# Performance work log

Hardware: AMD Instinct MI355X
Metric: run time of the kernel (lower is better)

The kernel has to match this reference:

```python
import jax, jax.numpy as jnp
import numpy as np

B, S, L, D = 4, 8, 350, 768  # paragraphs, sentences/paragraph, padded pair length, hidden
P = B * S * (S - 1)          # number of ordered sentence pairs = 224

# pair p -> (z, j, k): same enumeration order as the torch nested loops
_IDX = np.array([(z, j, k) for z in range(B) for j in range(S) for k in range(S) if j != k])
# each pair contributes its first-sentence embedding to segment (z,j) and second to (z,k)
_SEG = np.stack([_IDX[:, 0] * S + _IDX[:, 1], _IDX[:, 0] * S + _IDX[:, 2]], axis=1).reshape(-1)  # [2P]


def setup_inputs() -> dict:
    key = jax.random.key(0)
    ks = jax.random.split(key, 8)
    sc = 0.02
    all_output = jax.random.normal(ks[0], (P, L, D), dtype=jnp.float32)
    first_sep = jax.random.randint(ks[1], (P,), 5, 150).astype(jnp.int32)           # > 1
    second_sep = (first_sep + jax.random.randint(ks[2], (P,), 5, 150)).astype(jnp.int32)  # > first_sep+1, < L
    W1 = jax.random.normal(ks[3], (D, D), dtype=jnp.float32) * sc
    b1 = jnp.zeros((D,), jnp.float32)
    v1 = jax.random.normal(ks[4], (D,), dtype=jnp.float32) * sc
    vb1 = jnp.zeros((), jnp.float32)
    W2 = jax.random.normal(ks[5], (D, D), dtype=jnp.float32) * sc
    b2 = jnp.zeros((D,), jnp.float32)
    v2 = jax.random.normal(ks[6], (D,), dtype=jnp.float32) * sc
    vb2 = jnp.zeros((), jnp.float32)
    return {"all_output": all_output, "first_sep": first_sep, "second_sep": second_sep,
            "W1": W1, "b1": b1, "v1": v1, "vb1": vb1,
            "W2": W2, "b2": b2, "v2": v2, "vb2": vb2}


def reference(all_output, first_sep, second_sep, W1, b1, v1, vb1, W2, b2, v2, vb2):
    # pair_embeddings = [CLS] token of every pair
    pair_embeddings = all_output[:, 0, :]  # [P, D]

    # ---- level one: masked attention pooling over word positions ----
    u = jnp.tanh(all_output @ W1 + b1)          # [P, L, D]
    scores = u @ v1 + vb1                       # [P, L]
    pos = jnp.arange(L)[None, :]                # [1, L]
    mask1 = (pos >= 1) & (pos < first_sep[:, None])                 # tokens 1..first_sep-1
    mask2 = (pos > first_sep[:, None]) & (pos < second_sep[:, None])  # first_sep+1..second_sep-1

    def pool(mask):
        s = jnp.where(mask, scores, -jnp.inf)
        w = jax.nn.softmax(s, axis=1)           # [P, L]
        return jnp.einsum('pl,pld->pd', w, all_output)

    e1 = pool(mask1)                            # [P, D] first-sentence embeddings
    e2 = pool(mask2)                            # [P, D] second-sentence embeddings
    emb = jnp.stack([e1, e2], axis=1).reshape(2 * P, D)  # [2P, D]

    # ---- level two: segment attention pooling per (paragraph, sentence) group ----
    seg = jnp.asarray(_SEG)                     # [2P] segment ids, num_segments = B*S
    u2 = jnp.tanh(emb @ W2 + b2)                # [2P, D]
    sc = u2 @ v2 + vb2                          # [2P]
    num_seg = B * S
    smax = jax.ops.segment_max(sc, seg, num_segments=num_seg)
    ex = jnp.exp(sc - smax[seg])
    denom = jax.ops.segment_sum(ex, seg, num_segments=num_seg)
    w = ex / denom[seg]                         # segment softmax weights
    out2 = jax.ops.segment_sum(w[:, None] * emb, seg, num_segments=num_seg).reshape(B, S, D)
    return (pair_embeddings, out2)
```

## Files before the change

kernel.cpp:

```cpp
#include <hip/hip_runtime.h>
#include <math.h>

#define LSEQ   350
#define DDIM   768
#define NPAIR  224
#define MROWS1 78400
#define NSLAB1 613
#define MAXSLAB 520

typedef short bf16x8 __attribute__((ext_vector_type(8)));
typedef float f32x4  __attribute__((ext_vector_type(4)));

typedef const unsigned int __attribute__((address_space(1)))* gas_ptr;
typedef unsigned int __attribute__((address_space(3)))* las_ptr;

__device__ __forceinline__ void gload_lds16(const void* g, void* l) {
  __builtin_amdgcn_global_load_lds((gas_ptr)g, (las_ptr)l, 16, 0, 0);
}

__device__ __forceinline__ unsigned short f2bf(float x) {
  unsigned int u = __float_as_uint(x);
  unsigned int r = (u + 0x7FFFu + ((u >> 16) & 1u)) >> 16;
  return (unsigned short)r;
}

__device__ __forceinline__ float tanh_fast(float x) {
  float e = __expf(2.f * x);
  return 1.f - 2.f / (e + 1.f);
}

__global__ __launch_bounds__(256) void k_scan(const int* __restrict__ ssep,
                                              int* __restrict__ off) {
  __shared__ int buf[256];
  const int t = threadIdx.x;
  int v = (t < NPAIR) ? (ssep[t] - 1) : 0;
  buf[t] = v;
  __syncthreads();
#pragma unroll
  for (int d = 1; d < 256; d <<= 1) {
    int add = (t >= d) ? buf[t - d] : 0;
    __syncthreads();
    buf[t] += add;
    __syncthreads();
  }
  if (t < NPAIR) off[t] = buf[t] - v;
  if (t == NPAIR - 1) off[NPAIR] = buf[t];
}

__global__ __launch_bounds__(256) void k_wt2(const float* __restrict__ W1,
                                             const float* __restrict__ W2,
                                             unsigned short* __restrict__ Wt1,
                                             unsigned short* __restrict__ Wt2) {
  const float* W = blockIdx.z ? W2 : W1;
  unsigned short* Wt = blockIdx.z ? Wt2 : Wt1;
  __shared__ float tile[32][33];
  int bk = blockIdx.x * 32, bn = blockIdx.y * 32;
  int tx = threadIdx.x & 31, ty = threadIdx.x >> 5;
#pragma unroll
  for (int i = 0; i < 32; i += 8)
    tile[ty + i][tx] = W[(size_t)(bk + ty + i) * DDIM + bn + tx];
  __syncthreads();
#pragma unroll
  for (int i = 0; i < 32; i += 8)
    Wt[(size_t)(bn + ty + i) * DDIM + bk + tx] = f2bf(tile[tx][ty + i]);
}

__global__ __launch_bounds__(256) void k_w1t(const float* __restrict__ W,
                                             unsigned short* __restrict__ Wt) {
  __shared__ float tile[32][33];
  int bk = blockIdx.x * 32, bn = blockIdx.y * 32;
  int tx = threadIdx.x & 31, ty = threadIdx.x >> 5;
#pragma unroll
  for (int i = 0; i < 32; i += 8)
    tile[ty + i][tx] = W[(size_t)(bk + ty + i) * DDIM + bn + tx];
  __syncthreads();
#pragma unroll
  for (int i = 0; i < 32; i += 8)
    Wt[(size_t)(bn + ty + i) * DDIM + bk + tx] = f2bf(tile[tx][ty + i]);
}

__global__ __launch_bounds__(256) void k_conv(const float* __restrict__ X,
                                              const int* __restrict__ ssep,
                                              const int* __restrict__ off,
                                              unsigned short* __restrict__ Xbf,
                                              int* __restrict__ rowmap) {
  const int p = blockIdx.x, tile = blockIdx.y, z = blockIdx.z;
  const int nrow = ssep[p] - 1;
  const int r0 = tile * 128 + z * 32;
  if (r0 >= nrow) return;
  const int t = threadIdx.x;
  const int o = off[p];
  if (t < 192) {
    for (int i = 0; i < 32; ++i) {
      int r = r0 + i;
      if (r >= nrow) break;
      float4 x = *(const float4*)(X + ((size_t)p * LSEQ + 1 + r) * DDIM + t * 4);
      unsigned int ux = __float_as_uint(x.x) + 0x8000u;
      unsigned int uy = __float_as_uint(x.y) + 0x8000u;
      unsigned int uz = __float_as_uint(x.z) + 0x8000u;
      unsigned int uw = __float_as_uint(x.w) + 0x8000u;
      *(uint2*)(Xbf + (size_t)(o + r) * DDIM + t * 4) =
          make_uint2(__builtin_amdgcn_perm(uy, ux, 0x07060302u),
                     __builtin_amdgcn_perm(uw, uz, 0x07060302u));
    }
  } else if (t < 224) {
    int r = r0 + (t - 192);
    if (r < nrow) rowmap[o + r] = p * LSEQ + 1 + r;
  }
}

__global__ __launch_bounds__(256, 4) void k_gemm_c(
    const unsigned short* __restrict__ Xbf, const unsigned short* __restrict__ Wt,
    const float* __restrict__ bias, const float* __restrict__ vv,
    const int* __restrict__ off, const int* __restrict__ rowmap,
    float* __restrict__ scores) {
  const int Mtotal = off[NPAIR];
  const int b = blockIdx.x;
  const int g = b / 48, r = b - g * 48;
  const int slab = g * 8 + (r & 7);
  const int nchunk = r >> 3;
  if (slab * 128 >= Mtotal) return;

  const size_t arow0 = (size_t)slab * 128;
  const int n0 = nchunk * 128;

  __shared__ unsigned short As[128 * 32];
  __shared__ unsigned short Bs[128 * 32];

  const int t = threadIdx.x;
  const int lane = t & 63, w = t >> 6;
  const int l15 = t & 15;
  const int quad = (t >> 4) & 3;
  const int wm = w >> 1, wn = w & 1;
  const int lrow = lane >> 2;
  const int lcol = (lane & 3) * 8;

  f32x4 acc[4][4];
#pragma unroll
  for (int mi = 0; mi < 4; ++mi)
#pragma unroll
    for (int ni = 0; ni < 4; ++ni)
#pragma unroll
      for (int q = 0; q < 4; ++q) acc[mi][ni][q] = 0.f;

  for (int k0 = 0; k0 < DDIM; k0 += 32) {
#pragma unroll
    for (int j = 0; j < 2; ++j) {
      int seg = w * 2 + j;
      gload_lds16(Xbf + (arow0 + seg * 16 + lrow) * DDIM + k0 + lcol, As + seg * 512);
      gload_lds16(Wt + (size_t)(n0 + seg * 16 + lrow) * DDIM + k0 + lcol, Bs + seg * 512);
    }
    __syncthreads();

    bf16x8 a[4], bfr[4];
#pragma unroll
    for (int mi = 0; mi < 4; ++mi)
      a[mi] = *(const bf16x8*)&As[(wm * 64 + mi * 16 + l15) * 32 + quad * 8];
#pragma unroll
    for (int ni = 0; ni < 4; ++ni)
      bfr[ni] = *(const bf16x8*)&Bs[(wn * 64 + ni * 16 + l15) * 32 + quad * 8];
#pragma unroll
    for (int mi = 0; mi < 4; ++mi)
#pragma unroll
      for (int ni = 0; ni < 4; ++ni)
        acc[mi][ni] = __builtin_amdgcn_mfma_f32_16x16x32_bf16(a[mi], bfr[ni], acc[mi][ni], 0, 0, 0);
    __syncthreads();
  }

  float vvv[4], bbv[4];
#pragma unroll
  for (int ni = 0; ni < 4; ++ni) {
    int n = n0 + wn * 64 + ni * 16 + l15;
    vvv[ni] = vv[n];
    bbv[ni] = bias[n];
  }
#pragma unroll
  for (int mi = 0; mi < 4; ++mi) {
#pragma unroll
    for (int reg = 0; reg < 4; ++reg) {
      float s = 0.f;
#pragma unroll
      for (int ni = 0; ni < 4; ++ni)
        s += tanh_fast(acc[mi][ni][reg] + bbv[ni]) * vvv[ni];
      s += __shfl_xor(s, 1);
      s += __shfl_xor(s, 2);
      s += __shfl_xor(s, 4);
      s += __shfl_xor(s, 8);
      if (l15 == mi * 4 + reg) {
        int row = (int)arow0 + wm * 64 + mi * 16 + quad * 4 + reg;
        if (row < Mtotal) atomicAdd(&scores[rowmap[row]], s);
      }
    }
  }
}

__global__ __launch_bounds__(256, 2) void k_gemm_score(
    const float* __restrict__ X, const unsigned short* __restrict__ Wt,
    const float* __restrict__ bias, const float* __restrict__ vv,
    float* __restrict__ outs, int Mrows, int swz) {
  int slab, nchunk;
  if (swz) {
    int b = blockIdx.x;
    int g = b / 48, r = b - g * 48;
    slab = g * 8 + (r & 7);
    nchunk = r >> 3;
    if (slab >= NSLAB1) return;
  } else {
    slab = blockIdx.y;
    nchunk = blockIdx.x;
  }
  const int row0 = slab * 128;
  const int n0 = nchunk * 128;

  __shared__ unsigned short As[128][40];
  __shared__ unsigned short Bs[128][40];

  const int t = threadIdx.x;
  const int l15 = t & 15;
  const int quad = (t >> 4) & 3;
  const int w = t >> 6;
  const int wm = w >> 1, wn = w & 1;
  const int ar = t >> 3;
  const int ac = (t & 7) * 4;
  const int br = t >> 2;
  const int bc = (t & 3) * 8;

  f32x4 acc[4][4];
#pragma unroll
  for (int mi = 0; mi < 4; ++mi)
#pragma unroll
    for (int ni = 0; ni < 4; ++ni)
#pragma unroll
      for (int q = 0; q < 4; ++q) acc[mi][ni][q] = 0.f;

  for (int k0 = 0; k0 < DDIM; k0 += 32) {
#pragma unroll
    for (int pass = 0; pass < 4; ++pass) {
      int rr = ar + pass * 32;
      int row = row0 + rr;
      float4 x = make_float4(0.f, 0.f, 0.f, 0.f);
      if (row < Mrows) x = *(const float4*)(X + (size_t)row * DDIM + k0 + ac);
      unsigned int ux = __float_as_uint(x.x) + 0x8000u;
      unsigned int uy = __float_as_uint(x.y) + 0x8000u;
      unsigned int uz = __float_as_uint(x.z) + 0x8000u;
      unsigned int uw = __float_as_uint(x.w) + 0x8000u;
      *(uint2*)&As[rr][ac] = make_uint2(__builtin_amdgcn_perm(uy, ux, 0x07060302u),
                                        __builtin_amdgcn_perm(uw, uz, 0x07060302u));
    }
#pragma unroll
    for (int pp = 0; pp < 2; ++pp) {
      int rr = br + pp * 64;
      *(uint4*)&Bs[rr][bc] = *(const uint4*)(Wt + (size_t)(n0 + rr) * DDIM + k0 + bc);
    }
    __syncthreads();

    bf16x8 a[4], bfr[4];
#pragma unroll
    for (int mi = 0; mi < 4; ++mi)
      a[mi] = *(const bf16x8*)&As[wm * 64 + mi * 16 + l15][quad * 8];
#pragma unroll
    for (int ni = 0; ni < 4; ++ni)
      bfr[ni] = *(const bf16x8*)&Bs[wn * 64 + ni * 16 + l15][quad * 8];
#pragma unroll
    for (int mi = 0; mi < 4; ++mi)
#pragma unroll
      for (int ni = 0; ni < 4; ++ni)
        acc[mi][ni] = __builtin_amdgcn_mfma_f32_16x16x32_bf16(a[mi], bfr[ni], acc[mi][ni], 0, 0, 0);
    __syncthreads();
  }

  float vvv[4], bbv[4];
#pragma unroll
  for (int ni = 0; ni < 4; ++ni) {
    int n = n0 + wn * 64 + ni * 16 + l15;
    vvv[ni] = vv[n];
    bbv[ni] = bias[n];
  }
#pragma unroll
  for (int mi = 0; mi < 4; ++mi) {
#pragma unroll
    for (int reg = 0; reg < 4; ++reg) {
      float s = 0.f;
#pragma unroll
      for (int ni = 0; ni < 4; ++ni)
        s += tanh_fast(acc[mi][ni][reg] + bbv[ni]) * vvv[ni];
      s += __shfl_xor(s, 1);
      s += __shfl_xor(s, 2);
      s += __shfl_xor(s, 4);
      s += __shfl_xor(s, 8);
      if (l15 == mi * 4 + reg) {
        int row = row0 + wm * 64 + mi * 16 + quad * 4 + reg;
        if (row < Mrows) atomicAdd(&outs[row], s);
      }
    }
  }
}

__device__ __forceinline__ float block_reduce(float v, bool is_max, float* redbuf) {
#pragma unroll
  for (int off = 1; off < 64; off <<= 1) {
    float o = __shfl_xor(v, off);
    v = is_max ? fmaxf(v, o) : (v + o);
  }
  int wv = threadIdx.x >> 6;
  if ((threadIdx.x & 63) == 0) redbuf[wv] = v;
  __syncthreads();
  float r = is_max ? fmaxf(fmaxf(redbuf[0], redbuf[1]), fmaxf(redbuf[2], redbuf[3]))
                   : (redbuf[0] + redbuf[1] + redbuf[2] + redbuf[3]);
  __syncthreads();
  return r;
}

__global__ __launch_bounds__(256) void k_pool2(
    const unsigned short* __restrict__ Xbf, const float* __restrict__ X,
    const float* __restrict__ scores, const int* __restrict__ fsep,
    const int* __restrict__ ssep, const int* __restrict__ off,
    float* __restrict__ emb, float* __restrict__ out) {
  const int p = blockIdx.x, c = blockIdx.y, t = threadIdx.x;
  const int fs = fsep[p], ss = ssep[p];
  __shared__ float sw1[LSEQ], sw2[LSEQ];
  __shared__ float redbuf[4];

  float m1p = -INFINITY, m2p = -INFINITY;
  for (int l = t; l < LSEQ; l += 256) {
    float s = scores[p * LSEQ + l];
    float s1 = (l >= 1 && l < fs) ? s : -INFINITY;
    float s2 = (l > fs && l < ss) ? s : -INFINITY;
    sw1[l] = s1; sw2[l] = s2;
    m1p = fmaxf(m1p, s1); m2p = fmaxf(m2p, s2);
  }
  __syncthreads();
  float m1 = block_reduce(m1p, true, redbuf);
  float m2 = block_reduce(m2p, true, redbuf);
  float d1p = 0.f, d2p = 0.f;
  for (int l = t; l < LSEQ; l += 256) {
    float e1v = __expf(sw1[l] - m1);
    float e2v = __expf(sw2[l] - m2);
    sw1[l] = e1v; sw2[l] = e2v;
    d1p += e1v; d2p += e2v;
  }
  __syncthreads();
  float inv1 = 1.f / block_reduce(d1p, false, redbuf);
  float inv2 = 1.f / block_reduce(d2p, false, redbuf);

  if (c == 0 && t < 192) {
    *(float4*)(out + (size_t)p * DDIM + t * 4) =
        *(const float4*)(X + (size_t)p * LSEQ * DDIM + t * 4);
  }

  if (t < 192) {
    const int o = off[p];
    float A1[4] = {0.f, 0.f, 0.f, 0.f}, A2[4] = {0.f, 0.f, 0.f, 0.f};
    for (int l = 1 + c; l < ss; l += 8) {
      float wa = sw1[l] * inv1, wb = sw2[l] * inv2;
      uint2 xv = *(const uint2*)(Xbf + (size_t)(o + l - 1) * DDIM + t * 4);
      float x0 = __uint_as_float((xv.x & 0xFFFFu) << 16);
      float x1 = __uint_as_float(xv.x & 0xFFFF0000u);
      float x2 = __uint_as_float((xv.y & 0xFFFFu) << 16);
      float x3 = __uint_as_float(xv.y & 0xFFFF0000u);
      A1[0] += wa * x0; A1[1] += wa * x1; A1[2] += wa * x2; A1[3] += wa * x3;
      A2[0] += wb * x0; A2[1] += wb * x1; A2[2] += wb * x2; A2[3] += wb * x3;
    }
    float* e1 = emb + (size_t)(2 * p) * DDIM + t * 4;
    float* e2 = emb + (size_t)(2 * p + 1) * DDIM + t * 4;
#pragma unroll
    for (int i = 0; i < 4; ++i) atomicAdd(&e1[i], A1[i]);
#pragma unroll
    for (int i = 0; i < 4; ++i) atomicAdd(&e2[i], A2[i]);
  }
}

__global__ __launch_bounds__(256) void k_pool(
    const float* __restrict__ X, const float* __restrict__ scores,
    const int* __restrict__ fsep, const int* __restrict__ ssep,
    float* __restrict__ emb, float* __restrict__ out) {
  const int p = blockIdx.x;
  const int c = blockIdx.y;
  const int t = threadIdx.x;
  const int fs = fsep[p], ss = ssep[p];
  __shared__ float sw1[LSEQ], sw2[LSEQ];
  __shared__ float redbuf[4];

  float m1p = -INFINITY, m2p = -INFINITY;
  for (int l = t; l < LSEQ; l += 256) {
    float s = scores[p * LSEQ + l];
    float s1 = (l >= 1 && l < fs) ? s : -INFINITY;
    float s2 = (l > fs && l < ss) ? s : -INFINITY;
    sw1[l] = s1; sw2[l] = s2;
    m1p = fmaxf(m1p, s1); m2p = fmaxf(m2p, s2);
  }
  __syncthreads();
  float m1 = block_reduce(m1p, true, redbuf);
  float m2 = block_reduce(m2p, true, redbuf);
  float d1p = 0.f, d2p = 0.f;
  for (int l = t; l < LSEQ; l += 256) {
    float e1v = __expf(sw1[l] - m1);
    float e2v = __expf(sw2[l] - m2);
    sw1[l] = e1v; sw2[l] = e2v;
    d1p += e1v; d2p += e2v;
  }
  __syncthreads();
  float inv1 = 1.f / block_reduce(d1p, false, redbuf);
  float inv2 = 1.f / block_reduce(d2p, false, redbuf);
  const float* base = X + (size_t)p * LSEQ * DDIM;
  if (c == 0) {
    float* po = out + (size_t)p * DDIM;
    po[t] = base[t]; po[t + 256] = base[t + 256]; po[t + 512] = base[t + 512];
  }
  if (t < 192) {
    float4 A1 = make_float4(0.f, 0.f, 0.f, 0.f);
    float4 A2 = make_float4(0.f, 0.f, 0.f, 0.f);
    for (int l = 1 + c; l < ss; l += 8) {
      float wa = sw1[l] * inv1, wb = sw2[l] * inv2;
      float4 x = *(const float4*)(base + (size_t)l * DDIM + 4 * t);
      A1.x += wa * x.x; A1.y += wa * x.y; A1.z += wa * x.z; A1.w += wa * x.w;
      A2.x += wb * x.x; A2.y += wb * x.y; A2.z += wb * x.z; A2.w += wb * x.w;
    }
    float* e1 = emb + (size_t)(2 * p) * DDIM + 4 * t;
    float* e2 = emb + (size_t)(2 * p + 1) * DDIM + 4 * t;
    atomicAdd(&e1[0], A1.x); atomicAdd(&e1[1], A1.y);
    atomicAdd(&e1[2], A1.z); atomicAdd(&e1[3], A1.w);
    atomicAdd(&e2[0], A2.x); atomicAdd(&e2[1], A2.y);
    atomicAdd(&e2[2], A2.z); atomicAdd(&e2[3], A2.w);
  }
}

__global__ __launch_bounds__(256) void k_segout(
    const float* __restrict__ emb, const float* __restrict__ sc,
    float* __restrict__ out2) {
  const int g = blockIdx.x;
  const int z = g >> 3, j = g & 7;
  const int t = threadIdx.x;
  int ee[14];
#pragma unroll
  for (int i = 0; i < 7; ++i) ee[i] = 2 * (z * 56 + j * 7 + i);
#pragma unroll
  for (int i = 0; i < 7; ++i) {
    int j2 = i + (i >= j ? 1 : 0);
    int kk = j - (j > j2 ? 1 : 0);
    ee[7 + i] = 2 * (z * 56 + j2 * 7 + kk) + 1;
  }
  float sv[14];
  float m = -INFINITY;
#pragma unroll
  for (int i = 0; i < 14; ++i) { sv[i] = sc[ee[i]]; m = fmaxf(m, sv[i]); }
  float den = 0.f;
#pragma unroll
  for (int i = 0; i < 14; ++i) { sv[i] = __expf(sv[i] - m); den += sv[i]; }
  float inv = 1.f / den;
  float a0 = 0.f, a1 = 0.f, a2 = 0.f;
#pragma unroll
  for (int i = 0; i < 14; ++i) {
    float wgt = sv[i] * inv;
    const float* er = emb + (size_t)ee[i] * DDIM;
    a0 += wgt * er[t]; a1 += wgt * er[t + 256]; a2 += wgt * er[t + 512];
  }
  out2[(size_t)g * DDIM + t] = a0;
  out2[(size_t)g * DDIM + t + 256] = a1;
  out2[(size_t)g * DDIM + t + 512] = a2;
}

extern "C" void kernel_launch(void* const* d_in, const int* in_sizes, int n_in,
                              void* d_out, int out_size, void* d_ws, size_t ws_size,
                              hipStream_t stream) {
  const float* X  = (const float*)d_in[0];
  const int* fs   = (const int*)d_in[1];
  const int* ss   = (const int*)d_in[2];
  const float* W1 = (const float*)d_in[3];
  const float* b1 = (const float*)d_in[4];
  const float* v1 = (const float*)d_in[5];
  const float* W2 = (const float*)d_in[7];
  const float* b2 = (const float*)d_in[8];
  const float* v2 = (const float*)d_in[9];
  float* out = (float*)d_out;

  char* ws = (char*)d_ws;
  const size_t XBF_ROWS = (size_t)MAXSLAB * 128 + 64;
  const size_t OFF_MAP  = XBF_ROWS * DDIM * 2;
  const size_t OFF_OFF  = OFF_MAP + XBF_ROWS * 4;
  const size_t OFF_WT1  = OFF_OFF + 1024;
  const size_t OFF_WT2  = OFF_WT1 + 1179648;
  const size_t OFF_SCORES = OFF_WT2 + 1179648;
  const size_t OFF_EMB  = OFF_SCORES + 313600;
  const size_t OFF_SC   = OFF_EMB + 1376256;
  const size_t NEED     = OFF_SC + 2048;

  if (ws_size >= NEED) {
    unsigned short* Xbf = (unsigned short*)ws;
    int*   rowmap = (int*)(ws + OFF_MAP);
    int*   off    = (int*)(ws + OFF_OFF);
    unsigned short* Wt1 = (unsigned short*)(ws + OFF_WT1);
    unsigned short* Wt2 = (unsigned short*)(ws + OFF_WT2);
    float* scores = (float*)(ws + OFF_SCORES);
    float* emb    = (float*)(ws + OFF_EMB);
    float* sc     = (float*)(ws + OFF_SC);

    k_scan<<<1, 256, 0, stream>>>(ss, off);
    k_wt2<<<dim3(24, 24, 2), 256, 0, stream>>>(W1, W2, Wt1, Wt2);
    hipMemsetAsync(scores, 0, 313600 + 1376256 + 2048, stream);
    k_conv<<<dim3(NPAIR, 3, 4), 256, 0, stream>>>(X, ss, off, Xbf, rowmap);
    k_gemm_c<<<65 * 48, 256, 0, stream>>>(Xbf, Wt1, b1, v1, off, rowmap, scores);
    k_pool2<<<dim3(NPAIR, 8), 256, 0, stream>>>(Xbf, X, scores, fs, ss, off, emb, out);
    k_gemm_score<<<dim3(6, 4), 256, 0, stream>>>(emb, Wt2, b2, v2, sc, 448, 0);
    k_segout<<<32, 256, 0, stream>>>(emb, sc, out + (size_t)NPAIR * DDIM);
  } else {
    unsigned short* Wt = (unsigned short*)ws;
    float* scores = (float*)(ws + 1179648);
    float* emb    = (float*)(ws + 1493248);
    float* sc     = scores;

    k_w1t<<<dim3(24, 24), 256, 0, stream>>>(W1, Wt);
    hipMemsetAsync(scores, 0, MROWS1 * sizeof(float), stream);
    hipMemsetAsync(emb, 0, 448 * DDIM * sizeof(float), stream);
    k_gemm_score<<<77 * 48, 256, 0, stream>>>(X, Wt, b1, v1, scores, MROWS1, 1);
    k_pool<<<dim3(NPAIR, 8), 256, 0, stream>>>(X, scores, fs, ss, emb, out);
    k_w1t<<<dim3(24, 24), 256, 0, stream>>>(W2, Wt);
    hipMemsetAsync(sc, 0, 448 * sizeof(float), stream);
    k_gemm_score<<<dim3(6, 4), 256, 0, stream>>>(emb, Wt, b2, v2, sc, 448, 0);
    k_segout<<<32, 256, 0, stream>>>(emb, sc, out + (size_t)NPAIR * DDIM);
  }
}
```

Baseline: 500.0 us.

## Merge prep kernels, store compact scores, drop rowmap, and pool without atomics

Merges the scan, the weight transposes and the zeroing of the score buffer into one prep kernel, which removes separate launches and a memset. Scores are now stored compactly by row index, so the rowmap indirection goes away. The pooling kernel uses one block per pair over all positions and writes emb directly instead of using atomics, so emb no longer needs zeroing. This gives fewer launches and less atomic traffic, but pooling now has only 224 blocks, which lowers parallelism.

```diff
diff --git a/kernel.cpp b/kernel.cpp
--- a/kernel.cpp
+++ b/kernel.cpp
@@ -29,91 +29,79 @@
   return 1.f - 2.f / (e + 1.f);
 }
 
-__global__ __launch_bounds__(256) void k_scan(const int* __restrict__ ssep,
-                                              int* __restrict__ off) {
-  __shared__ int buf[256];
+#define PREP_WT 1152
+#define PREP_ZB 263
+__global__ __launch_bounds__(256) void k_prep(
+    const float* __restrict__ W1, const float* __restrict__ W2,
+    unsigned short* __restrict__ Wt1, unsigned short* __restrict__ Wt2,
+    const int* __restrict__ ssep, int* __restrict__ off,
+    unsigned int* __restrict__ zreg) {
+  const int b = blockIdx.x;
   const int t = threadIdx.x;
-  int v = (t < NPAIR) ? (ssep[t] - 1) : 0;
-  buf[t] = v;
-  __syncthreads();
-#pragma unroll
-  for (int d = 1; d < 256; d <<= 1) {
-    int add = (t >= d) ? buf[t - d] : 0;
+  if (b < PREP_WT) {
+    const float* W = (b >= 576) ? W2 : W1;
+    unsigned short* Wt = (b >= 576) ? Wt2 : Wt1;
+    const int r = (b >= 576) ? b - 576 : b;
+    const int bk = (r % 24) * 32, bn = (r / 24) * 32;
+    __shared__ float tile[32][33];
+    const int tx = t & 31, ty = t >> 5;
+#pragma unroll
+    for (int i = 0; i < 32; i += 8)
+      tile[ty + i][tx] = W[(size_t)(bk + ty + i) * DDIM + bn + tx];
     __syncthreads();
-    buf[t] += add;
+#pragma unroll
+    for (int i = 0; i < 32; i += 8)
+      Wt[(size_t)(bn + ty + i) * DDIM + bk + tx] = f2bf(tile[tx][ty + i]);
+  } else if (b == PREP_WT) {
+    __shared__ int buf[256];
+    int v = (t < NPAIR) ? (ssep[t] - 1) : 0;
+    buf[t] = v;
     __syncthreads();
-  }
-  if (t < NPAIR) off[t] = buf[t] - v;
-  if (t == NPAIR - 1) off[NPAIR] = buf[t];
-}
-
-__global__ __launch_bounds__(256) void k_wt2(const float* __restrict__ W1,
-                                             const float* __restrict__ W2,
-                                             unsigned short* __restrict__ Wt1,
-                                             unsigned short* __restrict__ Wt2) {
-  const float* W = blockIdx.z ? W2 : W1;
-  unsigned short* Wt = blockIdx.z ? Wt2 : Wt1;
-  __shared__ float tile[32][33];
-  int bk = blockIdx.x * 32, bn = blockIdx.y * 32;
-  int tx = threadIdx.x & 31, ty = threadIdx.x >> 5;
-#pragma unroll
-  for (int i = 0; i < 32; i += 8)
-    tile[ty + i][tx] = W[(size_t)(bk + ty + i) * DDIM + bn + tx];
-  __syncthreads();
-#pragma unroll
-  for (int i = 0; i < 32; i += 8)
-    Wt[(size_t)(bn + ty + i) * DDIM + bk + tx] = f2bf(tile[tx][ty + i]);
-}
-
-__global__ __launch_bounds__(256) void k_w1t(const float* __restrict__ W,
-                                             unsigned short* __restrict__ Wt) {
-  __shared__ float tile[32][33];
-  int bk = blockIdx.x * 32, bn = blockIdx.y * 32;
-  int tx = threadIdx.x & 31, ty = threadIdx.x >> 5;
-#pragma unroll
-  for (int i = 0; i < 32; i += 8)
-    tile[ty + i][tx] = W[(size_t)(bk + ty + i) * DDIM + bn + tx];
-  __syncthreads();
-#pragma unroll
-  for (int i = 0; i < 32; i += 8)
-    Wt[(size_t)(bn + ty + i) * DDIM + bk + tx] = f2bf(tile[tx][ty + i]);
-}
-
-__global__ __launch_bounds__(256) void k_conv(const float* __restrict__ X,
+#pragma unroll
+    for (int d = 1; d < 256; d <<= 1) {
+      int add = (t >= d) ? buf[t - d] : 0;
+      __syncthreads();
+      buf[t] += add;
+      __syncthreads();
+    }
+    if (t < NPAIR) off[t] = buf[t] - v;
+    if (t == NPAIR - 1) off[NPAIR] = buf[t];
+  } else {
+    const int i = b - PREP_WT - 1;
+    zreg[(size_t)i * 256 + t] = 0u;
+  }
+}
+
+__global__ __launch_bounds__(192) void k_conv(const float* __restrict__ X,
                                               const int* __restrict__ ssep,
                                               const int* __restrict__ off,
-                                              unsigned short* __restrict__ Xbf,
-                                              int* __restrict__ rowmap) {
+                                              unsigned short* __restrict__ Xbf) {
   const int p = blockIdx.x, tile = blockIdx.y, z = blockIdx.z;
   const int nrow = ssep[p] - 1;
   const int r0 = tile * 128 + z * 32;
   if (r0 >= nrow) return;
   const int t = threadIdx.x;
   const int o = off[p];
-  if (t < 192) {
-    for (int i = 0; i < 32; ++i) {
-      int r = r0 + i;
-      if (r >= nrow) break;
-      float4 x = *(const float4*)(X + ((size_t)p * LSEQ + 1 + r) * DDIM + t * 4);
-      unsigned int ux = __float_as_uint(x.x) + 0x8000u;
-      unsigned int uy = __float_as_uint(x.y) + 0x8000u;
-      unsigned int uz = __float_as_uint(x.z) + 0x8000u;
-      unsigned int uw = __float_as_uint(x.w) + 0x8000u;
-      *(uint2*)(Xbf + (size_t)(o + r) * DDIM + t * 4) =
-          make_uint2(__builtin_amdgcn_perm(uy, ux, 0x07060302u),
-                     __builtin_amdgcn_perm(uw, uz, 0x07060302u));
-    }
-  } else if (t < 224) {
-    int r = r0 + (t - 192);
-    if (r < nrow) rowmap[o + r] = p * LSEQ + 1 + r;
+  const int rmax = min(32, nrow - r0);
+  const float* src = X + ((size_t)p * LSEQ + 1 + r0) * DDIM + t * 4;
+  unsigned short* dst = Xbf + (size_t)(o + r0) * DDIM + t * 4;
+#pragma unroll 4
+  for (int i = 0; i < rmax; ++i) {
+    float4 x = *(const float4*)(src + (size_t)i * DDIM);
+    unsigned int ux = __float_as_uint(x.x) + 0x8000u;
+    unsigned int uy = __float_as_uint(x.y) + 0x8000u;
+    unsigned int uz = __float_as_uint(x.z) + 0x8000u;
+    unsigned int uw = __float_as_uint(x.w) + 0x8000u;
+    *(uint2*)(dst + (size_t)i * DDIM) =
+        make_uint2(__builtin_amdgcn_perm(uy, ux, 0x07060302u),
+                   __builtin_amdgcn_perm(uw, uz, 0x07060302u));
   }
 }
 
 __global__ __launch_bounds__(256, 4) void k_gemm_c(
     const unsigned short* __restrict__ Xbf, const unsigned short* __restrict__ Wt,
     const float* __restrict__ bias, const float* __restrict__ vv,
-    const int* __restrict__ off, const int* __restrict__ rowmap,
-    float* __restrict__ scores) {
+    const int* __restrict__ off, float* __restrict__ scores_c) {
   const int Mtotal = off[NPAIR];
   const int b = blockIdx.x;
   const int g = b / 48, r = b - g * 48;
@@ -188,7 +176,7 @@
       s += __shfl_xor(s, 8);
       if (l15 == mi * 4 + reg) {
         int row = (int)arow0 + wm * 64 + mi * 16 + quad * 4 + reg;
-        if (row < Mtotal) atomicAdd(&scores[rowmap[row]], s);
+        if (row < Mtotal) atomicAdd(&scores_c[row], s);
       }
     }
   }
@@ -311,19 +299,20 @@
   return r;
 }
 
-__global__ __launch_bounds__(256) void k_pool2(
+__global__ __launch_bounds__(256) void k_pool3(
     const unsigned short* __restrict__ Xbf, const float* __restrict__ X,
-    const float* __restrict__ scores, const int* __restrict__ fsep,
+    const float* __restrict__ scores_c, const int* __restrict__ fsep,
     const int* __restrict__ ssep, const int* __restrict__ off,
     float* __restrict__ emb, float* __restrict__ out) {
-  const int p = blockIdx.x, c = blockIdx.y, t = threadIdx.x;
+  const int p = blockIdx.x, t = threadIdx.x;
   const int fs = fsep[p], ss = ssep[p];
+  const int o = off[p];
   __shared__ float sw1[LSEQ], sw2[LSEQ];
   __shared__ float redbuf[4];
 
   float m1p = -INFINITY, m2p = -INFINITY;
   for (int l = t; l < LSEQ; l += 256) {
-    float s = scores[p * LSEQ + l];
+    float s = (l >= 1 && l < ss) ? scores_c[o + l - 1] : 0.f;
     float s1 = (l >= 1 && l < fs) ? s : -INFINITY;
     float s2 = (l > fs && l < ss) ? s : -INFINITY;
     sw1[l] = s1; sw2[l] = s2;
@@ -343,17 +332,16 @@
   float inv1 = 1.f / block_reduce(d1p, false, redbuf);
   float inv2 = 1.f / block_reduce(d2p, false, redbuf);
 
-  if (c == 0 && t < 192) {
+  if (t < 192) {
     *(float4*)(out + (size_t)p * DDIM + t * 4) =
         *(const float4*)(X + (size_t)p * LSEQ * DDIM + t * 4);
-  }
-
-  if (t < 192) {
-    const int o = off[p];
+
     float A1[4] = {0.f, 0.f, 0.f, 0.f}, A2[4] = {0.f, 0.f, 0.f, 0.f};
-    for (int l = 1 + c; l < ss; l += 8) {
+    const unsigned short* xb = Xbf + (size_t)o * DDIM + t * 4;
+#pragma unroll 2
+    for (int l = 1; l < ss; ++l) {
       float wa = sw1[l] * inv1, wb = sw2[l] * inv2;
-      uint2 xv = *(const uint2*)(Xbf + (size_t)(o + l - 1) * DDIM + t * 4);
+      uint2 xv = *(const uint2*)(xb + (size_t)(l - 1) * DDIM);
       float x0 = __uint_as_float((xv.x & 0xFFFFu) << 16);
       float x1 = __uint_as_float(xv.x & 0xFFFF0000u);
       float x2 = __uint_as_float((xv.y & 0xFFFFu) << 16);
@@ -361,13 +349,25 @@
       A1[0] += wa * x0; A1[1] += wa * x1; A1[2] += wa * x2; A1[3] += wa * x3;
       A2[0] += wb * x0; A2[1] += wb * x1; A2[2] += wb * x2; A2[3] += wb * x3;
     }
-    float* e1 = emb + (size_t)(2 * p) * DDIM + t * 4;
-    float* e2 = emb + (size_t)(2 * p + 1) * DDIM + t * 4;
-#pragma unroll
-    for (int i = 0; i < 4; ++i) atomicAdd(&e1[i], A1[i]);
-#pragma unroll
-    for (int i = 0; i < 4; ++i) atomicAdd(&e2[i], A2[i]);
-  }
+    *(float4*)(emb + (size_t)(2 * p) * DDIM + t * 4) =
+        make_float4(A1[0], A1[1], A1[2], A1[3]);
+    *(float4*)(emb + (size_t)(2 * p + 1) * DDIM + t * 4) =
+        make_float4(A2[0], A2[1], A2[2], A2[3]);
+  }
+}
+
+__global__ __launch_bounds__(256) void k_w1t(const float* __restrict__ W,
+                                             unsigned short* __restrict__ Wt) {
+  __shared__ float tile[32][33];
+  int bk = blockIdx.x * 32, bn = blockIdx.y * 32;
+  int tx = threadIdx.x & 31, ty = threadIdx.x >> 5;
+#pragma unroll
+  for (int i = 0; i < 32; i += 8)
+    tile[ty + i][tx] = W[(size_t)(bk + ty + i) * DDIM + bn + tx];
+  __syncthreads();
+#pragma unroll
+  for (int i = 0; i < 32; i += 8)
+    Wt[(size_t)(bn + ty + i) * DDIM + bk + tx] = f2bf(tile[tx][ty + i]);
 }
 
 __global__ __launch_bounds__(256) void k_pool(
@@ -475,32 +475,30 @@
   float* out = (float*)d_out;
 
   char* ws = (char*)d_ws;
-  const size_t XBF_ROWS = (size_t)MAXSLAB * 128 + 64;
-  const size_t OFF_MAP  = XBF_ROWS * DDIM * 2;
-  const size_t OFF_OFF  = OFF_MAP + XBF_ROWS * 4;
+  const size_t XBF_ROWS = (size_t)MAXSLAB * 128 + 128;
+  const size_t OFF_OFF  = XBF_ROWS * DDIM * 2;
   const size_t OFF_WT1  = OFF_OFF + 1024;
   const size_t OFF_WT2  = OFF_WT1 + 1179648;
-  const size_t OFF_SCORES = OFF_WT2 + 1179648;
-  const size_t OFF_EMB  = OFF_SCORES + 313600;
-  const size_t OFF_SC   = OFF_EMB + 1376256;
-  const size_t NEED     = OFF_SC + 2048;
+  const size_t OFF_SCC  = OFF_WT2 + 1179648;
+  const size_t OFF_SC2  = OFF_SCC + 266752;
+  const size_t ZBYTES   = (size_t)PREP_ZB * 1024;
+  const size_t OFF_EMB  = OFF_SCC + ZBYTES;
+  const size_t NEED     = OFF_EMB + 1376256;
 
   if (ws_size >= NEED) {
     unsigned short* Xbf = (unsigned short*)ws;
-    int*   rowmap = (int*)(ws + OFF_MAP);
-    int*   off    = (int*)(ws + OFF_OFF);
+    int*   off     = (int*)(ws + OFF_OFF);
     unsigned short* Wt1 = (unsigned short*)(ws + OFF_WT1);
     unsigned short* Wt2 = (unsigned short*)(ws + OFF_WT2);
-    float* scores = (float*)(ws + OFF_SCORES);
-    float* emb    = (float*)(ws + OFF_EMB);
-    float* sc     = (float*)(ws + OFF_SC);
-
-    k_scan<<<1, 256, 0, stream>>>(ss, off);
-    k_wt2<<<dim3(24, 24, 2), 256, 0, stream>>>(W1, W2, Wt1, Wt2);
-    hipMemsetAsync(scores, 0, 313600 + 1376256 + 2048, stream);
-    k_conv<<<dim3(NPAIR, 3, 4), 256, 0, stream>>>(X, ss, off, Xbf, rowmap);
-    k_gemm_c<<<65 * 48, 256, 0, stream>>>(Xbf, Wt1, b1, v1, off, rowmap, scores);
-    k_pool2<<<dim3(NPAIR, 8), 256, 0, stream>>>(Xbf, X, scores, fs, ss, off, emb, out);
+    float* scores_c = (float*)(ws + OFF_SCC);
+    float* sc       = (float*)(ws + OFF_SC2);
+    float* emb      = (float*)(ws + OFF_EMB);
+
+    k_prep<<<PREP_WT + 1 + PREP_ZB, 256, 0, stream>>>(
+        W1, W2, Wt1, Wt2, ss, off, (unsigned int*)scores_c);
+    k_conv<<<dim3(NPAIR, 3, 4), 192, 0, stream>>>(X, ss, off, Xbf);
+    k_gemm_c<<<65 * 48, 256, 0, stream>>>(Xbf, Wt1, b1, v1, off, scores_c);
+    k_pool3<<<NPAIR, 256, 0, stream>>>(Xbf, X, scores_c, fs, ss, off, emb, out);
     k_gemm_score<<<dim3(6, 4), 256, 0, stream>>>(emb, Wt2, b2, v2, sc, 448, 0);
     k_segout<<<32, 256, 0, stream>>>(emb, sc, out + (size_t)NPAIR * DDIM);
   } else {
```

After: 489.1 us. 1.02x faster.
